# Performance work log

Measured on AMD Instinct MI355X. Metric: run time of the kernel, lower is better.

The kernel has to match this reference:

```python
import jax, jax.numpy as jnp
import numpy as np

N_NODES = 100000
IN_CH, HID_CH, OUT_CH = 128, 128, 64
N_EDGES = 1600000


def gcn_conv(x, W, b, src, dst, num_nodes):
    """PyG GCNConv: x@W -> symmetric-normalized aggregation with self-loops -> +bias."""
    h = x @ W  # [N, out]
    loop = jnp.arange(num_nodes, dtype=src.dtype)
    src_a = jnp.concatenate([src, loop])  # add self-loops
    dst_a = jnp.concatenate([dst, loop])
    # degree of destination nodes over augmented edge set (edge_weight = 1)
    deg = jax.ops.segment_sum(jnp.ones_like(dst_a, dtype=h.dtype), dst_a,
                              num_segments=num_nodes)
    dis = jnp.where(deg > 0, jax.lax.rsqrt(jnp.maximum(deg, 1e-30)), 0.0)
    norm = dis[src_a] * dis[dst_a]  # [E+N]
    msg = h[src_a] * norm[:, None]  # gather + normalize
    out = jax.ops.segment_sum(msg, dst_a, num_segments=num_nodes)  # scatter-add
    return out + b


def setup_inputs() -> dict:
    key = jax.random.key(0)
    ks = jax.random.split(key, 9)
    x = jax.random.normal(ks[0], (N_NODES, IN_CH), dtype=jnp.float32)
    edge_index = jax.random.randint(ks[1], (2, N_EDGES), 0, N_NODES, dtype=jnp.int64)
    def glorot(k, fan_in, fan_out):
        s = np.sqrt(6.0 / (fan_in + fan_out)).astype(np.float32)
        return jax.random.uniform(k, (fan_in, fan_out), jnp.float32, -s, s)
    return {
        "x": x,
        "edge_index": edge_index,
        "W1": glorot(ks[2], IN_CH, HID_CH),
        "b1": jnp.zeros((HID_CH,), jnp.float32),
        "W2": glorot(ks[3], HID_CH, HID_CH),
        "b2": jnp.zeros((HID_CH,), jnp.float32),
        "Wo": glorot(ks[4], HID_CH, OUT_CH),
        "bo": jnp.zeros((OUT_CH,), jnp.float32),
    }


def reference(x, edge_index, W1, b1, W2, b2, Wo, bo):
    src, dst = edge_index[0], edge_index[1]
    n = x.shape[0]
    x1 = jax.nn.relu(gcn_conv(x, W1, b1, src, dst, n))
    x2 = jax.nn.relu(gcn_conv(x1, W2, b2, src, dst, n))
    return (x1 + x2) @ Wo + bo
```

## Files before the change

### kernel.cpp

```cpp
#include <hip/hip_runtime.h>
#include <hip/hip_fp16.h>

#define N_NODES 100000
#define N_EDGES 1600000
#define CH 128
#define OCH 64
#define NBUCKET 391
#define CAP 8192
#define BIN_CHUNK 4096
#define ZROW N_NODES
#define GG 782

typedef _Float16 half8 __attribute__((ext_vector_type(8)));
typedef float f32x4 __attribute__((ext_vector_type(4)));

__device__ __forceinline__ ushort f2h(float f) {
    _Float16 h = (_Float16)f;
    return *(ushort*)&h;
}

__device__ __forceinline__ uint pkadd(uint a, uint b) {
    __half2 r = __hadd2(*(__half2*)&a, *(__half2*)&b);
    return *(uint*)&r;
}

__device__ __forceinline__ uint4 pk4(uint4 a, uint4 b) {
    a.x = pkadd(a.x, b.x); a.y = pkadd(a.y, b.y);
    a.z = pkadd(a.z, b.z); a.w = pkadd(a.w, b.w);
    return a;
}

__device__ __forceinline__ int swz(int row, int k) {
    return row * 128 + ((((k >> 3) ^ (row & 15)) << 3) | (k & 7));
}


__global__ __launch_bounds__(512) void k_bin_prep(const int* __restrict__ src,
                                                  const int* __restrict__ dst,
                                                  int* __restrict__ bfill,
                                                  int* __restrict__ bin,
                                                  const float* __restrict__ W1,
                                                  const float* __restrict__ W2,
                                                  const float* __restrict__ Wo,
                                                  ushort* __restrict__ W1s,
                                                  ushort* __restrict__ W2s,
                                                  ushort* __restrict__ WoTs,
                                                  ushort* __restrict__ h,
                                                  ushort* __restrict__ h2) {
    __shared__ int hist[512];
    __shared__ int excl[512];
    __shared__ int wbase[512];
    __shared__ int cur[512];
    __shared__ int sbuf[BIN_CHUNK];
    __shared__ ushort sbkt[BIN_CHUNK];
    const int t = threadIdx.x;

    if (blockIdx.x >= NBUCKET) {
        int b = blockIdx.x - NBUCKET;
        if (b == 80) {
            if (t < CH) {
                h[(size_t)ZROW * CH + t] = 0;
                h2[(size_t)ZROW * CH + t] = 0;
            }
        } else {
            int i = b * 512 + t;
            if (i < 16384) {
                int k = i >> 7, n = i & 127;
                W1s[swz(n, k)] = f2h(W1[i]);
            } else if (i < 32768) {
                int j = i - 16384, k = j >> 7, n = j & 127;
                W2s[swz(n, k)] = f2h(W2[j]);
            } else {
                int j = i - 32768, k = j >> 6, n = j & 63;
                WoTs[swz(n, k)] = f2h(Wo[j]);
            }
        }
        return;
    }

    const int e0 = blockIdx.x * BIN_CHUNK;
    hist[t] = 0;
    __syncthreads();

    int ss[8], bb[8], dl[8];
#pragma unroll
    for (int j = 0; j < 8; ++j) {
        int e = e0 + j * 512 + t;
        bb[j] = -1;
        if (e < N_EDGES) {
            int s = src[e], d = dst[e];
            ss[j] = s; dl[j] = d & 255; bb[j] = d >> 8;
            atomicAdd(&hist[bb[j]], 1);
        }
    }
    __syncthreads();

    int v = hist[t];
    for (int off = 1; off < 512; off <<= 1) {
        int tv = (t >= off) ? hist[t - off] : 0;
        __syncthreads();
        hist[t] += tv;
        __syncthreads();
    }
    int ex = hist[t] - v;
    excl[t] = ex;
    cur[t] = ex;
    if (t < NBUCKET && v > 0) wbase[t] = atomicAdd(&bfill[t], v);
    __syncthreads();

#pragma unroll
    for (int j = 0; j < 8; ++j) {
        if (bb[j] >= 0) {
            int p = atomicAdd(&cur[bb[j]], 1);
            sbuf[p] = (ss[j] << 8) | dl[j];
            sbkt[p] = (ushort)bb[j];
        }
    }
    const int nloc = hist[511];
    __syncthreads();

    for (int i = t; i < nloc; i += 512) {
        int b = sbkt[i];
        bin[b * CAP + wbase[b] + (i - excl[b])] = sbuf[i];
    }
}


__global__ __launch_bounds__(512) void k_build(const int* __restrict__ bfill,
                                               const int* __restrict__ bin,
                                               int* __restrict__ esrc,
                                               int2* __restrict__ scnt,
                                               float* __restrict__ dis) {
    __shared__ int pre[512];
    __shared__ int cnt_l[256];
    __shared__ int cur_l[256];
    __shared__ int sortbuf[CAP];
    const int t = threadIdx.x;
    const int b = blockIdx.x;

    pre[t] = (t < NBUCKET) ? bfill[t] : 0;
    if (t < 256) cnt_l[t] = 0;
    __syncthreads();
    for (int off = 1; off < 512; off <<= 1) {
        int tv = (t >= off) ? pre[t - off] : 0;
        __syncthreads();
        pre[t] += tv;
        __syncthreads();
    }
    const int n = bfill[b];
    const int base = pre[b] - n;
    const int* brec = bin + b * CAP;

    for (int i = t; i < n; i += 512)
        atomicAdd(&cnt_l[brec[i] & 255], 1);
    __syncthreads();

    int v = (t < 256) ? cnt_l[t] : 0;
    for (int off = 1; off < 256; off <<= 1) {
        int tv = (t >= off && t < 256) ? cnt_l[t - off] : 0;
        __syncthreads();
        if (t < 256) cnt_l[t] += tv;
        __syncthreads();
    }
    if (t < 256) {
        int excl = cnt_l[t] - v;
        int node = b * 256 + t;
        if (node < N_NODES) {
            scnt[node] = make_int2(base + excl, v);
            dis[node] = rsqrtf((float)(v + 1));
        }
        cur_l[t] = excl;
    }
    __syncthreads();

    for (int i = t; i < n; i += 512) {
        int rec = brec[i];
        int p = atomicAdd(&cur_l[rec & 255], 1);
        sortbuf[p] = rec >> 8;
    }
    __syncthreads();
    for (int i = t; i < n; i += 512)
        esrc[base + i] = sortbuf[i];
}


__global__ __launch_bounds__(512) void k_gemm_mfma(const float* __restrict__ A,
                                                   const ushort* __restrict__ Ws,
                                                   const float* __restrict__ dis,
                                                   ushort* __restrict__ out) {
    __shared__ ushort sB[128 * 128];
    __shared__ ushort sA[128 * 136];
    const int tid = threadIdx.x;
    const int row0 = blockIdx.x * 128;

    for (int i = tid; i < 2048; i += 512)
        ((float4*)sB)[i] = ((const float4*)Ws)[i];

    for (int i = tid; i < 4096; i += 512) {
        int m = i >> 5, u = i & 31, k4 = u << 2;
        int r = row0 + m;
        ushort4 pk = make_ushort4(0, 0, 0, 0);
        if (r < N_NODES) {
            float4 a = ((const float4*)A)[r * 32 + u];
            pk = make_ushort4(f2h(a.x), f2h(a.y), f2h(a.z), f2h(a.w));
        }
        *(ushort4*)&sA[swz(m, k4)] = pk;
    }
    __syncthreads();

    const int lane = tid & 63, wv = tid >> 6;
    const int mrow = lane & 15, quad = lane >> 4;
    f32x4 acc[8] = {};
#pragma unroll
    for (int kc = 0; kc < 4; ++kc) {
        int g = kc * 4 + quad;
        half8 a = *(const half8*)&sA[(wv * 16 + mrow) * 128 + ((g ^ mrow) << 3)];
#pragma unroll
        for (int nt = 0; nt < 8; ++nt) {
            half8 b = *(const half8*)&sB[(nt * 16 + mrow) * 128 + ((g ^ mrow) << 3)];
            acc[nt] = __builtin_amdgcn_mfma_f32_16x16x32_f16(a, b, acc[nt], 0, 0, 0);
        }
    }

    const int rbase4 = wv * 16 + quad * 4;
    float ds[4];
#pragma unroll
    for (int rg = 0; rg < 4; ++rg) {
        int r = row0 + rbase4 + rg;
        ds[rg] = (r < N_NODES) ? dis[r] : 0.f;
    }

    __syncthreads();
#pragma unroll
    for (int nt = 0; nt < 8; ++nt) {
#pragma unroll
        for (int rg = 0; rg < 4; ++rg)
            sA[(rbase4 + rg) * 136 + nt * 16 + mrow] = f2h(acc[nt][rg] * ds[rg]);
    }
    __syncthreads();

#pragma unroll
    for (int k = 0; k < 4; ++k) {
        int idx = tid + k * 512;
        int m = idx >> 4, c16 = idx & 15;
        int r = row0 + m;
        if (r < N_NODES) {
            uint4 vv = *(const uint4*)&sA[m * 136 + c16 * 8];
            ((uint4*)out)[(size_t)r * 16 + c16] = vv;
        }
    }
}


struct Ictx { int n; int grp; int s0, s1, s2, s3, s4, s5; };
struct Gt { uint4 t0, t1, t2, t3, t4, t5, slf; };

__device__ __forceinline__ Ictx idx_stage(const int* __restrict__ esrc, int off, int n, int q) {
    Ictx c; c.n = n;
    const int* ep = esrc + off;
    int r0 = ep[q], r1 = ep[q + 4], r2 = ep[q + 8];
    int r3 = ep[q + 12], r4 = ep[q + 16], r5 = ep[q + 20];
    bool grp = (q + 12 < n);
    bool ok = (n <= q + 24);
    c.grp = grp;
    c.s0 = (grp || q < n)      ? r0 : ZROW;
    c.s1 = (grp || q + 4 < n)  ? r1 : ZROW;
    c.s2 = (grp || q + 8 < n)  ? r2 : ZROW;
    c.s3 = grp                 ? r3 : ZROW;
    c.s4 = (grp && ok && q + 16 < n) ? r4 : ZROW;
    c.s5 = (grp && ok && q + 20 < n) ? r5 : ZROW;
    return c;
}

__device__ __forceinline__ Gt gather_stage(const Ictx& c, int v, int l,
                                           const uint4* __restrict__ h16) {
    Gt g;
    g.t0 = h16[(size_t)c.s0 * 16 + l];
    g.t1 = h16[(size_t)c.s1 * 16 + l];
    g.t2 = h16[(size_t)c.s2 * 16 + l];
    g.t3 = h16[(size_t)c.s3 * 16 + l];
    g.t4 = h16[(size_t)c.s4 * 16 + l];
    g.t5 = h16[(size_t)c.s5 * 16 + l];
    g.slf = h16[(size_t)v * 16 + l];
    return g;
}

__device__ __forceinline__ uint4 acc_reduce(const Gt& g, const Ictx& c, int q, int l,
                                            const int* __restrict__ esrc, int off,
                                            const uint4* __restrict__ h16,
                                            float dsv, float4 b0, float4 b1) {
    uint4 aA = make_uint4(0, 0, 0, 0), aB = make_uint4(0, 0, 0, 0);
    aA = pk4(aA, g.t0);
    if (c.grp) aB = pk4(aB, g.t1); else aA = pk4(aA, g.t1);
    aA = pk4(aA, g.t2);
    if (c.grp) aB = pk4(aB, g.t3); else aA = pk4(aA, g.t3);
    aA = pk4(aA, g.t4);
    aA = pk4(aA, g.t5);
    if (c.n > q + 24) {
        const int* ep = esrc + off;
        int i = q + 16;
        for (; i + 12 < c.n; i += 16) {
            uint4 u0 = h16[(size_t)ep[i] * 16 + l];
            uint4 u1 = h16[(size_t)ep[i + 4] * 16 + l];
            uint4 u2 = h16[(size_t)ep[i + 8] * 16 + l];
            uint4 u3 = h16[(size_t)ep[i + 12] * 16 + l];
            aA = pk4(aA, u0); aB = pk4(aB, u1); aA = pk4(aA, u2); aB = pk4(aB, u3);
        }
        for (; i < c.n; i += 4) aA = pk4(aA, h16[(size_t)ep[i] * 16 + l]);
    }
    aA = pk4(aA, aB);
    aA.x = pkadd(aA.x, (uint)__shfl_xor((int)aA.x, 16));
    aA.y = pkadd(aA.y, (uint)__shfl_xor((int)aA.y, 16));
    aA.z = pkadd(aA.z, (uint)__shfl_xor((int)aA.z, 16));
    aA.w = pkadd(aA.w, (uint)__shfl_xor((int)aA.w, 16));
    aA.x = pkadd(aA.x, (uint)__shfl_xor((int)aA.x, 32));
    aA.y = pkadd(aA.y, (uint)__shfl_xor((int)aA.y, 32));
    aA.z = pkadd(aA.z, (uint)__shfl_xor((int)aA.z, 32));
    aA.w = pkadd(aA.w, (uint)__shfl_xor((int)aA.w, 32));

    aA = pk4(aA, g.slf);
    float2 a0 = __half22float2(*(__half2*)&aA.x);
    float2 a1 = __half22float2(*(__half2*)&aA.y);
    float2 a2 = __half22float2(*(__half2*)&aA.z);
    float2 a3 = __half22float2(*(__half2*)&aA.w);
    a0.x = fmaxf(a0.x * dsv + b0.x, 0.f); a0.y = fmaxf(a0.y * dsv + b0.y, 0.f);
    a1.x = fmaxf(a1.x * dsv + b0.z, 0.f); a1.y = fmaxf(a1.y * dsv + b0.w, 0.f);
    a2.x = fmaxf(a2.x * dsv + b1.x, 0.f); a2.y = fmaxf(a2.y * dsv + b1.y, 0.f);
    a3.x = fmaxf(a3.x * dsv + b1.z, 0.f); a3.y = fmaxf(a3.y * dsv + b1.w, 0.f);
    __half2 o0 = __float22half2_rn(a0);
    __half2 o1 = __float22half2_rn(a1);
    __half2 o2 = __float22half2_rn(a2);
    __half2 o3 = __float22half2_rn(a3);
    return make_uint4(*(uint*)&o0, *(uint*)&o1, *(uint*)&o2, *(uint*)&o3);
}


__global__ __launch_bounds__(256) void k_agg_gemm(const int2* __restrict__ scnt,
                                                  const int* __restrict__ esrc,
                                                  const ushort* __restrict__ h,
                                                  const float* __restrict__ dis,
                                                  const float* __restrict__ bias,
                                                  const ushort* __restrict__ W2s,
                                                  ushort* __restrict__ x1,
                                                  ushort* __restrict__ h2) {
    __shared__ ushort tile[16 * 128];
    __shared__ ushort sBnc[16 * 136];
    const int t = threadIdx.x;
    const int w = t >> 6;
    const int vb0 = blockIdx.x * 16;
    const int vb = vb0 + w * 4;
    const int lane = t & 63, q = lane >> 4, l = lane & 15;
    const uint4* h16 = (const uint4*)h;

    int2 m0 = scnt[vb], m1 = scnt[vb + 1], m2 = scnt[vb + 2], m3 = scnt[vb + 3];
    float d0 = dis[vb], d1 = dis[vb + 1], d2 = dis[vb + 2], d3 = dis[vb + 3];
    float4 b0 = ((const float4*)bias)[2 * l];
    float4 b1 = ((const float4*)bias)[2 * l + 1];

    Ictx c0 = idx_stage(esrc, m0.x, m0.y, q);
    Gt g0 = gather_stage(c0, vb, l, h16);
    Ictx c1 = idx_stage(esrc, m1.x, m1.y, q);
    Gt g1 = gather_stage(c1, vb + 1, l, h16);
    Ictx c2 = idx_stage(esrc, m2.x, m2.y, q);
    uint4 ov = acc_reduce(g0, c0, q, l, esrc, m0.x, h16, d0, b0, b1);
    if (q == 0) {
        ((uint4*)x1)[(size_t)vb * 16 + l] = ov;
        *(uint4*)&tile[swz(w * 4 + 0, l * 8)] = ov;
    }
    Gt g2 = gather_stage(c2, vb + 2, l, h16);
    Ictx c3 = idx_stage(esrc, m3.x, m3.y, q);
    ov = acc_reduce(g1, c1, q, l, esrc, m1.x, h16, d1, b0, b1);
    if (q == 0) {
        ((uint4*)x1)[(size_t)(vb + 1) * 16 + l] = ov;
        *(uint4*)&tile[swz(w * 4 + 1, l * 8)] = ov;
    }
    Gt g3 = gather_stage(c3, vb + 3, l, h16);
    ov = acc_reduce(g2, c2, q, l, esrc, m2.x, h16, d2, b0, b1);
    if (q == 0) {
        ((uint4*)x1)[(size_t)(vb + 2) * 16 + l] = ov;
        *(uint4*)&tile[swz(w * 4 + 2, l * 8)] = ov;
    }
    ov = acc_reduce(g3, c3, q, l, esrc, m3.x, h16, d3, b0, b1);
    if (q == 0) {
        ((uint4*)x1)[(size_t)(vb + 3) * 16 + l] = ov;
        *(uint4*)&tile[swz(w * 4 + 3, l * 8)] = ov;
    }
    __syncthreads();

    const int mrow = lane & 15, quad = lane >> 4;
    f32x4 acc0 = {}, acc1 = {};
    const int nt0 = 2 * w, nt1 = 2 * w + 1;
#pragma unroll
    for (int kc = 0; kc < 4; ++kc) {
        int g = kc * 4 + quad;
        half8 a = *(const half8*)&tile[mrow * 128 + ((g ^ mrow) << 3)];
        half8 bf0 = *(const half8*)&W2s[(nt0 * 16 + mrow) * 128 + ((g ^ mrow) << 3)];
        half8 bf1 = *(const half8*)&W2s[(nt1 * 16 + mrow) * 128 + ((g ^ mrow) << 3)];
        acc0 = __builtin_amdgcn_mfma_f32_16x16x32_f16(a, bf0, acc0, 0, 0, 0);
        acc1 = __builtin_amdgcn_mfma_f32_16x16x32_f16(a, bf1, acc1, 0, 0, 0);
    }
    float ds[4];
#pragma unroll
    for (int rg = 0; rg < 4; ++rg)
        ds[rg] = dis[vb0 + quad * 4 + rg];
#pragma unroll
    for (int rg = 0; rg < 4; ++rg) {
        sBnc[(quad * 4 + rg) * 136 + nt0 * 16 + mrow] = f2h(acc0[rg] * ds[rg]);
        sBnc[(quad * 4 + rg) * 136 + nt1 * 16 + mrow] = f2h(acc1[rg] * ds[rg]);
    }
    __syncthreads();

    int row = t >> 4, c16 = t & 15;
    uint4 vv = *(const uint4*)&sBnc[row * 136 + c16 * 8];
    ((uint4*)h2)[(size_t)(vb0 + row) * 16 + c16] = vv;
}


__global__ __launch_bounds__(256) void k_agg_out(const int2* __restrict__ scnt,
                                                 const int* __restrict__ esrc,
                                                 const ushort* __restrict__ h2,
                                                 const float* __restrict__ dis,
                                                 const float* __restrict__ bias,
                                                 const ushort* __restrict__ WoTs,
                                                 const float* __restrict__ bo,
                                                 const ushort* __restrict__ x1,
                                                 float* __restrict__ out) {
    __shared__ ushort tile[16 * 128];
    __shared__ float sOut[16 * 68];
    const int t = threadIdx.x;
    const int w = t >> 6;
    const int vb0 = blockIdx.x * 16;
    const int vb = vb0 + w * 4;
    const int lane = t & 63, q = lane >> 4, l = lane & 15;
    const uint4* h16 = (const uint4*)h2;
    const uint4* x1q = (const uint4*)x1;

    int2 m0 = scnt[vb], m1 = scnt[vb + 1], m2 = scnt[vb + 2], m3 = scnt[vb + 3];
    float d0 = dis[vb], d1 = dis[vb + 1], d2 = dis[vb + 2], d3 = dis[vb + 3];
    float4 b0 = ((const float4*)bias)[2 * l];
    float4 b1 = ((const float4*)bias)[2 * l + 1];

    Ictx c0 = idx_stage(esrc, m0.x, m0.y, q);
    Gt g0 = gather_stage(c0, vb, l, h16);
    uint4 xr0 = x1q[(size_t)vb * 16 + l];
    Ictx c1 = idx_stage(esrc, m1.x, m1.y, q);
    Gt g1 = gather_stage(c1, vb + 1, l, h16);
    uint4 xr1 = x1q[(size_t)(vb + 1) * 16 + l];
    Ictx c2 = idx_stage(esrc, m2.x, m2.y, q);
    uint4 ov = acc_reduce(g0, c0, q, l, esrc, m0.x, h16, d0, b0, b1);
    if (q == 0) *(uint4*)&tile[swz(w * 4 + 0, l * 8)] = pk4(ov, xr0);
    Gt g2 = gather_stage(c2, vb + 2, l, h16);
    uint4 xr2 = x1q[(size_t)(vb + 2) * 16 + l];
    Ictx c3 = idx_stage(esrc, m3.x, m3.y, q);
    uint4 xr3 = x1q[(size_t)(vb + 3) * 16 + l];
    ov = acc_reduce(g1, c1, q, l, esrc, m1.x, h16, d1, b0, b1);
    if (q == 0) *(uint4*)&tile[swz(w * 4 + 1, l * 8)] = pk4(ov, xr1);
    Gt g3 = gather_stage(c3, vb + 3, l, h16);
    ov = acc_reduce(g2, c2, q, l, esrc, m2.x, h16, d2, b0, b1);
    if (q == 0) *(uint4*)&tile[swz(w * 4 + 2, l * 8)] = pk4(ov, xr2);
    ov = acc_reduce(g3, c3, q, l, esrc, m3.x, h16, d3, b0, b1);
    if (q == 0) *(uint4*)&tile[swz(w * 4 + 3, l * 8)] = pk4(ov, xr3);
    __syncthreads();

    const int mrow = lane & 15, quad = lane >> 4;
    f32x4 acc = {};
#pragma unroll
    for (int kc = 0; kc < 4; ++kc) {
        int g = kc * 4 + quad;
        half8 a = *(const half8*)&tile[mrow * 128 + ((g ^ mrow) << 3)];
        half8 bf = *(const half8*)&WoTs[(w * 16 + mrow) * 128 + ((g ^ mrow) << 3)];
        acc = __builtin_amdgcn_mfma_f32_16x16x32_f16(a, bf, acc, 0, 0, 0);
    }
    float bb = bo[w * 16 + mrow];
#pragma unroll
    for (int rg = 0; rg < 4; ++rg)
        sOut[(quad * 4 + rg) * 68 + w * 16 + mrow] = acc[rg] + bb;
    __syncthreads();

    int row = t >> 4, c16 = t & 15;
    uint4 vv = *(const uint4*)&sOut[row * 68 + c16 * 4];
    ((uint4*)out)[(size_t)(vb0 + row) * 16 + c16] = vv;
}


extern "C" void kernel_launch(void* const* d_in, const int* in_sizes, int n_in,
                              void* d_out, int out_size, void* d_ws, size_t ws_size,
                              hipStream_t stream) {
    const float* x  = (const float*)d_in[0];
    const int*   ei = (const int*)d_in[1];
    const int*   src = ei;
    const int*   dst = ei + N_EDGES;
    const float* W1 = (const float*)d_in[2];
    const float* b1 = (const float*)d_in[3];
    const float* W2 = (const float*)d_in[4];
    const float* b2 = (const float*)d_in[5];
    const float* Wo = (const float*)d_in[6];
    const float* bo = (const float*)d_in[7];
    float* out = (float*)d_out;

    char* ws = (char*)d_ws;
    int*    bfill  = (int*)ws;            ws += 2048;
    int2*   scnt   = (int2*)ws;           ws += 800000;
    float*  dis    = (float*)ws;          ws += 400000;
    int*    bin    = (int*)ws;            ws += (size_t)NBUCKET * CAP * 4;
    int*    esrc   = (int*)ws;            ws += (size_t)N_EDGES * 4;
    ushort* W1s    = (ushort*)ws;         ws += 32768;
    ushort* W2s    = (ushort*)ws;         ws += 32768;
    ushort* WoTs   = (ushort*)ws;         ws += 16384;
    ushort* h      = (ushort*)ws;         ws += (size_t)(N_NODES + 1) * CH * 2;
    ushort* x1     = (ushort*)ws;         ws += (size_t)N_NODES * CH * 2;
    ushort* h2     = (ushort*)ws;

    const int gA = N_NODES / 16;

    hipMemsetAsync(bfill, 0, 2048, stream);
    k_bin_prep<<<NBUCKET + 81, 512, 0, stream>>>(src, dst, bfill, bin,
                                                 W1, W2, Wo, W1s, W2s, WoTs, h, h2);
    k_build<<<NBUCKET, 512, 0, stream>>>(bfill, bin, esrc, scnt, dis);

    k_gemm_mfma<<<GG, 512, 0, stream>>>(x, W1s, dis, h);

    k_agg_gemm<<<gA, 256, 0, stream>>>(scnt, esrc, h, dis, b1, W2s, x1, h2);

    k_agg_out<<<gA, 256, 0, stream>>>(scnt, esrc, h2, dis, b2, WoTs, bo, x1, out);
}
```

Before: 277.3 us.

## Fuse first-layer GEMM into CSR build kernel, reusing shared memory

```diff
diff --git a/kernel.cpp b/kernel.cpp
--- a/kernel.cpp
+++ b/kernel.cpp
@@ -9,7 +9,6 @@
 #define CAP 8192
 #define BIN_CHUNK 4096
 #define ZROW N_NODES
-#define GG 782
 
 typedef _Float16 half8 __attribute__((ext_vector_type(8)));
 typedef float f32x4 __attribute__((ext_vector_type(4)));
@@ -126,15 +125,20 @@
 }
 
 
-__global__ __launch_bounds__(512) void k_build(const int* __restrict__ bfill,
-                                               const int* __restrict__ bin,
-                                               int* __restrict__ esrc,
-                                               int2* __restrict__ scnt,
-                                               float* __restrict__ dis) {
+__global__ __launch_bounds__(512) void k_build_gemm(const int* __restrict__ bfill,
+                                                    const int* __restrict__ bin,
+                                                    int* __restrict__ esrc,
+                                                    int2* __restrict__ scnt,
+                                                    float* __restrict__ dis,
+                                                    const float* __restrict__ A,
+                                                    const ushort* __restrict__ W1s,
+                                                    ushort* __restrict__ hout) {
     __shared__ int pre[512];
     __shared__ int cnt_l[256];
     __shared__ int cur_l[256];
-    __shared__ int sortbuf[CAP];
+    __shared__ __align__(16) char smem[34816];
+    int* sortbuf = (int*)smem;
+    ushort* sA = (ushort*)smem;
     const int t = threadIdx.x;
     const int b = blockIdx.x;
 
@@ -181,73 +185,66 @@
     __syncthreads();
     for (int i = t; i < n; i += 512)
         esrc[base + i] = sortbuf[i];
-}
-
-
-__global__ __launch_bounds__(512) void k_gemm_mfma(const float* __restrict__ A,
-                                                   const ushort* __restrict__ Ws,
-                                                   const float* __restrict__ dis,
-                                                   ushort* __restrict__ out) {
-    __shared__ ushort sB[128 * 128];
-    __shared__ ushort sA[128 * 136];
-    const int tid = threadIdx.x;
-    const int row0 = blockIdx.x * 128;
-
-    for (int i = tid; i < 2048; i += 512)
-        ((float4*)sB)[i] = ((const float4*)Ws)[i];
-
-    for (int i = tid; i < 4096; i += 512) {
-        int m = i >> 5, u = i & 31, k4 = u << 2;
-        int r = row0 + m;
-        ushort4 pk = make_ushort4(0, 0, 0, 0);
-        if (r < N_NODES) {
-            float4 a = ((const float4*)A)[r * 32 + u];
-            pk = make_ushort4(f2h(a.x), f2h(a.y), f2h(a.z), f2h(a.w));
-        }
-        *(ushort4*)&sA[swz(m, k4)] = pk;
-    }
-    __syncthreads();
-
-    const int lane = tid & 63, wv = tid >> 6;
+    __syncthreads();
+
+    const int lane = t & 63, wv = t >> 6;
     const int mrow = lane & 15, quad = lane >> 4;
-    f32x4 acc[8] = {};
-#pragma unroll
-    for (int kc = 0; kc < 4; ++kc) {
-        int g = kc * 4 + quad;
-        half8 a = *(const half8*)&sA[(wv * 16 + mrow) * 128 + ((g ^ mrow) << 3)];
+#pragma unroll
+    for (int tile = 0; tile < 2; ++tile) {
+        const int row0 = b * 256 + tile * 128;
+
+        for (int i = t; i < 4096; i += 512) {
+            int m = i >> 5, u = i & 31, k4 = u << 2;
+            int r = row0 + m;
+            ushort4 pk = make_ushort4(0, 0, 0, 0);
+            if (r < N_NODES) {
+                float4 a = ((const float4*)A)[r * 32 + u];
+                pk = make_ushort4(f2h(a.x), f2h(a.y), f2h(a.z), f2h(a.w));
+            }
+            *(ushort4*)&sA[swz(m, k4)] = pk;
+        }
+        __syncthreads();
+
+        f32x4 acc[8] = {};
+#pragma unroll
+        for (int kc = 0; kc < 4; ++kc) {
+            int g = kc * 4 + quad;
+            half8 a = *(const half8*)&sA[(wv * 16 + mrow) * 128 + ((g ^ mrow) << 3)];
+#pragma unroll
+            for (int nt = 0; nt < 8; ++nt) {
+                half8 bf = *(const half8*)&W1s[(nt * 16 + mrow) * 128 + ((g ^ mrow) << 3)];
+                acc[nt] = __builtin_amdgcn_mfma_f32_16x16x32_f16(a, bf, acc[nt], 0, 0, 0);
+            }
+        }
+
+        const int rbase4 = wv * 16 + quad * 4;
+        float ds[4];
+#pragma unroll
+        for (int rg = 0; rg < 4; ++rg) {
+            int r = row0 + rbase4 + rg;
+            ds[rg] = (r < N_NODES) ? dis[r] : 0.f;
+        }
+
+        __syncthreads();
 #pragma unroll
         for (int nt = 0; nt < 8; ++nt) {
-            half8 b = *(const half8*)&sB[(nt * 16 + mrow) * 128 + ((g ^ mrow) << 3)];
-            acc[nt] = __builtin_amdgcn_mfma_f32_16x16x32_f16(a, b, acc[nt], 0, 0, 0);
-        }
-    }
-
-    const int rbase4 = wv * 16 + quad * 4;
-    float ds[4];
-#pragma unroll
-    for (int rg = 0; rg < 4; ++rg) {
-        int r = row0 + rbase4 + rg;
-        ds[rg] = (r < N_NODES) ? dis[r] : 0.f;
-    }
-
-    __syncthreads();
-#pragma unroll
-    for (int nt = 0; nt < 8; ++nt) {
-#pragma unroll
-        for (int rg = 0; rg < 4; ++rg)
-            sA[(rbase4 + rg) * 136 + nt * 16 + mrow] = f2h(acc[nt][rg] * ds[rg]);
-    }
-    __syncthreads();
-
-#pragma unroll
-    for (int k = 0; k < 4; ++k) {
-        int idx = tid + k * 512;
-        int m = idx >> 4, c16 = idx & 15;
-        int r = row0 + m;
-        if (r < N_NODES) {
-            uint4 vv = *(const uint4*)&sA[m * 136 + c16 * 8];
-            ((uint4*)out)[(size_t)r * 16 + c16] = vv;
-        }
+#pragma unroll
+            for (int rg = 0; rg < 4; ++rg)
+                sA[(rbase4 + rg) * 136 + nt * 16 + mrow] = f2h(acc[nt][rg] * ds[rg]);
+        }
+        __syncthreads();
+
+#pragma unroll
+        for (int k = 0; k < 4; ++k) {
+            int idx = t + k * 512;
+            int m = idx >> 4, c16 = idx & 15;
+            int r = row0 + m;
+            if (r < N_NODES) {
+                uint4 vv = *(const uint4*)&sA[m * 136 + c16 * 8];
+                ((uint4*)hout)[(size_t)r * 16 + c16] = vv;
+            }
+        }
+        __syncthreads();
     }
 }
 
@@ -516,11 +513,7 @@
     hipMemsetAsync(bfill, 0, 2048, stream);
     k_bin_prep<<<NBUCKET + 81, 512, 0, stream>>>(src, dst, bfill, bin,
                                                  W1, W2, Wo, W1s, W2s, WoTs, h, h2);
-    k_build<<<NBUCKET, 512, 0, stream>>>(bfill, bin, esrc, scnt, dis);
-
-    k_gemm_mfma<<<GG, 512, 0, stream>>>(x, W1s, dis, h);
-
+    k_build_gemm<<<NBUCKET, 512, 0, stream>>>(bfill, bin, esrc, scnt, dis, x, W1s, h);
     k_agg_gemm<<<gA, 256, 0, stream>>>(scnt, esrc, h, dis, b1, W2s, x1, h2);
-
     k_agg_out<<<gA, 256, 0, stream>>>(scnt, esrc, h2, dis, b2, WoTs, bo, x1, out);
 }
```

After: 281.9 us. No clear change (+1.6%).
